# Performance work log

Measured on AMD Instinct MI355X. Metric: run time of the kernel, lower is better.

Reference implementation:

```python
import jax, jax.numpy as jnp
from jax import lax
import numpy as np

B, N, E, U = 128, 1024, 300, 128
L = 512          # num_leaves per sample
NN = 2 * L - 1   # num_nodes per sample (binary tree)


def _hsig(x):
    # Keras hard_sigmoid: clip(0.2*x + 0.5, 0, 1)
    return jnp.clip(0.2 * x + 0.5, 0.0, 1.0)


def setup_inputs() -> dict:
    key = jax.random.key(0)
    ks = jax.random.split(key, 5)
    rng = np.random.default_rng(0)
    # children of node t are uniform in [0, t) -> valid bottom-up binary tree
    u = rng.random((B, N, 2))
    child = (u * np.arange(N)[None, :, None]).astype(np.int32)
    child[:, :L, :] = 0  # leaves have no children (never read)
    num_vecs = np.tile(np.array([[NN, L]], np.int32), (B, 1))
    return {
        "initial_state": jax.random.normal(ks[0], (B, N, E), jnp.float32),
        "translation_kernel": jax.random.normal(ks[1], (E, U), jnp.float32) * 0.05,
        "kernel": jax.random.normal(ks[2], (5 * U, U), jnp.float32) * 0.05,
        "recurrent_kernel": jax.random.normal(ks[3], (5 * U, 2 * U), jnp.float32) * 0.05,
        "bias": jnp.zeros((5 * U, 1), jnp.float32),
        "child_vecs": jnp.asarray(child),
        "num_vecs": jnp.asarray(num_vecs),
    }


def reference(initial_state, translation_kernel, kernel, recurrent_kernel, bias,
              child_vecs, num_vecs):
    b, n, _ = initial_state.shape
    units = kernel.shape[1]
    # leaf initial states: relu(x @ W_translate)  -> [B, N, U]
    x = jax.nn.relu(jnp.einsum('bne,eu->bnu', initial_state, translation_kernel))
    num_nodes = num_vecs[:, 0]
    num_leaves = num_vecs[:, 1]
    bvec = bias[:, 0][None, :]  # [1, 5U]

    def step(carry, t):
        H, C = carry  # [B, N, U] each
        ch = jnp.take(child_vecs, t, axis=1)                                   # [B, 2]
        h_ch = jnp.take_along_axis(H, ch[:, :, None], axis=1).reshape(b, 2 * units)
        c_ch = jnp.take_along_axis(C, ch[:, :, None], axis=1).reshape(b, 2 * units)
        xt = jnp.take(x, t, axis=1)                                            # [B, U]
        # z = kernel @ x^T + recurrent_kernel @ [h_l; h_r] + bias  (batched, [B, 5U])
        z = xt @ kernel.T + h_ch @ recurrent_kernel.T + bvec
        i = _hsig(z[:, :units])
        f = _hsig(z[:, units:3 * units])                                       # [B, 2U]
        o = _hsig(z[:, 3 * units:4 * units])
        g = jnp.tanh(z[:, 4 * units:])
        # faithful to original: reshape (flat_mem*f) as [U, 2] row-major, sum axis 1
        c_new = (c_ch * f).reshape(b, units, 2).sum(axis=-1) + i * g
        h_new = o * jnp.tanh(c_new)
        act = ((t >= num_leaves) & (t < num_nodes))[:, None]                   # [B, 1]
        h_upd = jnp.where(act, h_new, jnp.take(H, t, axis=1))
        c_upd = jnp.where(act, c_new, jnp.take(C, t, axis=1))
        H = lax.dynamic_update_slice(H, h_upd[:, None, :], (0, t, 0))
        C = lax.dynamic_update_slice(C, c_upd[:, None, :], (0, t, 0))
        return (H, C), None

    # leaves start with hidden = memory = translated vec; internal nodes overwritten in order
    (H, _), _ = lax.scan(step, (x, x), jnp.arange(n))
    valid = (jnp.arange(n)[None, :] < num_nodes[:, None])[..., None]
    return H * valid.astype(H.dtype)
```

## Files before the change

### kernel.cpp

```cpp
#include <hip/hip_runtime.h>
#include <hip/hip_bf16.h>

#define B_ 128
#define N_ 1024
#define E_ 300
#define U_ 128
#define M_ (B_ * N_)
#define Z_ (5 * U_)
#define LMAXT 40
#define LPAR 20

typedef __attribute__((ext_vector_type(8))) short bf16x8;
typedef __attribute__((ext_vector_type(4))) float f32x4;
typedef _Float16 f16x4 __attribute__((ext_vector_type(4)));
typedef _Float16 f16x8 __attribute__((ext_vector_type(8)));

__device__ __forceinline__ short f2bf(float f) {
  unsigned u = __builtin_bit_cast(unsigned, f);
  u = (u + 0x7fffu + ((u >> 16) & 1u)) >> 16;
  return (short)u;
}

__device__ __forceinline__ float hsig(float z) {
  float v = __builtin_fmaf(z, 0.2f, 0.5f);
  v = v < 0.f ? 0.f : v;
  v = v > 1.f ? 1.f : v;
  return v;
}

__device__ __forceinline__ float tanh_fast(float x) {
  float p = __expf(2.f * x);
  return 1.f - 2.f * __builtin_amdgcn_rcpf(p + 1.f);
}

__device__ __forceinline__ unsigned pk2(float a, float b) {
  return __builtin_bit_cast(unsigned, __builtin_amdgcn_cvt_pkrtz(a, b));
}

__device__ __forceinline__ f16x8 pack8(float4 a, float4 b) {
  uint4 u;
  u.x = pk2(a.x, a.y);
  u.y = pk2(a.z, a.w);
  u.z = pk2(b.x, b.y);
  u.w = pk2(b.z, b.w);
  return __builtin_bit_cast(f16x8, u);
}

__global__ __launch_bounds__(256) void prep(
    const float* __restrict__ Wr, const float* __restrict__ Wk,
    const float* __restrict__ tk, _Float16* __restrict__ W16,
    _Float16* __restrict__ Wk16, _Float16* __restrict__ tkT16) {
  const int idx = blockIdx.x * 256 + threadIdx.x;
  if (idx < 163840) {
    W16[idx] = (_Float16)Wr[idx];
  } else if (idx < 245760) {
    const int i = idx - 163840;
    Wk16[i] = (_Float16)Wk[i];
  } else if (idx < 286720) {
    const int i = idx - 245760;
    const int n = i / 320, k = i - n * 320;
    tkT16[i] = (k < E_) ? (_Float16)tk[k * U_ + n] : (_Float16)0.f;
  }
}

__global__ __launch_bounds__(256) void x_gemm(
    const float* __restrict__ A, const float* __restrict__ W,
    float* __restrict__ H, float* __restrict__ C) {
  __shared__ __align__(16) short As[64][40];
  __shared__ __align__(16) short Ws[128][40];
  __shared__ __align__(16) _Float16 xls[64][136];
  const int tid = threadIdx.x;
  const int m0 = blockIdx.x * 64;
  f32x4 acc[8] = {};
  const int lane = tid & 63, wv = tid >> 6;
  const int lr = lane & 15, lg = lane >> 4;

  for (int kc = 0; kc < 10; ++kc) {
    const int k0 = kc * 32;
    {
      const int row = tid >> 2, kk = (tid & 3) * 8;
      const float* src = A + (size_t)(m0 + row) * E_ + k0 + kk;
      bf16x8 v;
      if (k0 + 32 <= E_) {
#pragma unroll
        for (int i = 0; i < 8; ++i) v[i] = f2bf(src[i]);
      } else {
#pragma unroll
        for (int i = 0; i < 8; ++i)
          v[i] = (k0 + kk + i < E_) ? f2bf(src[i]) : (short)0;
      }
      *(bf16x8*)&As[row][kk] = v;
    }
#pragma unroll
    for (int s = 0; s < 2; ++s) {
      const int slot = tid + s * 256;
      const int n = slot & 127, kg = slot >> 7;
      bf16x8 v;
      if (k0 + 32 <= E_) {
#pragma unroll
        for (int i = 0; i < 8; ++i) v[i] = f2bf(W[(k0 + kg * 8 + i) * U_ + n]);
      } else {
#pragma unroll
        for (int i = 0; i < 8; ++i) {
          const int k = k0 + kg * 8 + i;
          v[i] = (k < E_) ? f2bf(W[k * U_ + n]) : (short)0;
        }
      }
      *(bf16x8*)&Ws[n][kg * 8] = v;
    }
    __syncthreads();
    bf16x8 a = *(const bf16x8*)&As[wv * 16 + lr][lg * 8];
#pragma unroll
    for (int nt = 0; nt < 8; ++nt) {
      bf16x8 b = *(const bf16x8*)&Ws[nt * 16 + lr][lg * 8];
      acc[nt] = __builtin_amdgcn_mfma_f32_16x16x32_bf16(a, b, acc[nt], 0, 0, 0);
    }
    __syncthreads();
  }
#pragma unroll
  for (int nt = 0; nt < 8; ++nt) {
#pragma unroll
    for (int r = 0; r < 4; ++r) {
      float v = acc[nt][r];
      v = v > 0.f ? v : 0.f;
      xls[wv * 16 + lg * 4 + r][nt * 16 + lr] = (_Float16)v;
    }
  }
  __syncthreads();
  {
    const int row = tid >> 2, c0 = (tid & 3) * 32;
    const size_t base = (size_t)(m0 + row) * U_;
#pragma unroll
    for (int s = 0; s < 4; ++s) {
      const f16x8 v = *(const f16x8*)&xls[row][c0 + 8 * s];
      const float4 lo = {(float)v[0], (float)v[1], (float)v[2], (float)v[3]};
      const float4 hi4 = {(float)v[4], (float)v[5], (float)v[6], (float)v[7]};
      *(float4*)(H + base + c0 + 8 * s) = lo;
      *(float4*)(H + base + c0 + 8 * s + 4) = hi4;
      *(float4*)(C + base + c0 + 8 * s) = lo;
      *(float4*)(C + base + c0 + 8 * s + 4) = hi4;
    }
  }
}

__global__ __launch_bounds__(256) void xz_gemm(
    const float* __restrict__ X, const _Float16* __restrict__ Wk16,
    const float* __restrict__ bias, const int* __restrict__ nv,
    _Float16* __restrict__ XZ) {
  const int m0 = blockIdx.x * 64;
  {
    const int bb = m0 >> 10;
    const int t0 = m0 & (N_ - 1);
    const int nodes = nv[2 * bb], leaves = nv[2 * bb + 1];
    if (t0 + 64 <= leaves || t0 >= nodes) return;
  }
  __shared__ __align__(16) short As[64][40];
  __shared__ __align__(16) short Ws[128][40];
  __shared__ __align__(16) _Float16 xzls[64][136];
  const int tid = threadIdx.x;
  const int n0 = blockIdx.y * 128;
  f32x4 acc[8] = {};
  const int lane = tid & 63, wv = tid >> 6;
  const int lr = lane & 15, lg = lane >> 4;

  for (int kc = 0; kc < 4; ++kc) {
    const int k0 = kc * 32;
    {
      const int row = tid >> 2, kk = (tid & 3) * 8;
      const float* src = X + (size_t)(m0 + row) * U_ + k0 + kk;
      const float4 a0 = *(const float4*)src;
      const float4 a1 = *(const float4*)(src + 4);
      *(f16x8*)&As[row][kk] = pack8(a0, a1);
    }
#pragma unroll
    for (int s = 0; s < 2; ++s) {
      const int slot = tid + s * 256;
      const int n = slot >> 2, kk = (slot & 3) * 8;
      *(f16x8*)&Ws[n][kk] =
          *(const f16x8*)(Wk16 + (size_t)(n0 + n) * U_ + k0 + kk);
    }
    __syncthreads();
    f16x8 a = *(const f16x8*)&As[wv * 16 + lr][lg * 8];
#pragma unroll
    for (int nt = 0; nt < 8; ++nt) {
      f16x8 b = *(const f16x8*)&Ws[nt * 16 + lr][lg * 8];
      acc[nt] = __builtin_amdgcn_mfma_f32_16x16x32_f16(a, b, acc[nt], 0, 0, 0);
    }
    __syncthreads();
  }
#pragma unroll
  for (int nt = 0; nt < 8; ++nt) {
    const float bv = bias[n0 + nt * 16 + lr];
#pragma unroll
    for (int r = 0; r < 4; ++r)
      xzls[wv * 16 + lg * 4 + r][nt * 16 + lr] = (_Float16)(acc[nt][r] + bv);
  }
  __syncthreads();
  {
    const int row = tid >> 2, c0 = (tid & 3) * 32;
    _Float16* dst = XZ + (size_t)(m0 + row) * Z_ + n0 + c0;
#pragma unroll
    for (int s = 0; s < 4; ++s)
      *(f16x8*)(dst + 8 * s) = *(const f16x8*)&xzls[row][c0 + 8 * s];
  }
}

__global__ __launch_bounds__(512) void levelize(
    const int* __restrict__ child, const int* __restrict__ nv,
    unsigned char* __restrict__ lv, short* __restrict__ rank,
    int* __restrict__ cnt) {
  const int b = blockIdx.x;
  const int tid = threadIdx.x;
  int nodes = nv[2 * b];
  int leaves = nv[2 * b + 1];
  if (nodes > N_) nodes = N_;
  if (leaves < 0) leaves = 0;

  __shared__ short lvs[N_];
  __shared__ int chs[2 * N_];
  __shared__ int cnts[LMAXT];
  __shared__ int changed;

  for (int i = tid; i < N_; i += 512) lvs[i] = 0;
  for (int i = tid; i < 2 * N_; i += 512) chs[i] = child[(size_t)b * 2 * N_ + i];
  if (tid < LMAXT) cnts[tid] = 0;
  __syncthreads();

  int stable = 0;
  for (int s = 0; s < 64; ++s) {
    if (tid == 0) changed = 0;
    __syncthreads();
    int any = 0;
    for (int t = leaves + tid; t < nodes; t += 512) {
      const int c0 = chs[2 * t], c1 = chs[2 * t + 1];
      const int l0 = (c0 < t && c0 >= 0) ? lvs[c0] : 0;
      const int l1 = (c1 < t && c1 >= 0) ? lvs[c1] : 0;
      const int l = 1 + (l0 > l1 ? l0 : l1);
      if (l > (int)lvs[t]) { lvs[t] = (short)l; any = 1; }
    }
    if (any) changed = 1;
    __syncthreads();
    if (!changed) { stable = 1; break; }
  }
  if (!stable) {
    if (tid == 0) {
      for (int t = leaves; t < nodes; ++t) {
        const int c0 = chs[2 * t], c1 = chs[2 * t + 1];
        const int l0 = (c0 < t && c0 >= 0) ? lvs[c0] : 0;
        const int l1 = (c1 < t && c1 >= 0) ? lvs[c1] : 0;
        lvs[t] = (short)(1 + (l0 > l1 ? l0 : l1));
      }
    }
    __syncthreads();
  }

  for (int t = leaves + tid; t < nodes; t += 512) {
    int l = lvs[t];
    if (l > LMAXT - 1) l = LMAXT - 1;
    lv[b * N_ + t] = (unsigned char)l;
    if (l < LMAXT - 1) rank[b * N_ + t] = (short)atomicAdd(&cnts[l], 1);
  }
  __syncthreads();
  if (tid == 0) {
    for (int t = leaves; t < nodes; ++t)
      if ((int)lvs[t] >= LMAXT - 1) rank[b * N_ + t] = (short)(cnts[LMAXT - 1]++);
  }
  __syncthreads();
  if (tid < LMAXT) cnt[tid * 128 + b] = cnts[tid];
}

__global__ __launch_bounds__(64) void offsets(
    const int* __restrict__ cnt, int* __restrict__ pos, int* __restrict__ goff) {
  const int l = threadIdx.x;
  __shared__ int tot[LMAXT];
  if (l < LMAXT) {
    int s = 0;
    for (int b = 0; b < 128; ++b) {
      pos[l * 128 + b] = s;
      s += cnt[l * 128 + b];
    }
    tot[l] = s;
  }
  __syncthreads();
  if (l == 0) {
    int g = 0;
    for (int i = 0; i < LMAXT; ++i) { goff[i] = g; g += tot[i]; }
    goff[LMAXT] = g;
  }
  __syncthreads();
  if (l < LMAXT) {
    const int g = goff[l];
    for (int b = 0; b < 128; ++b) pos[l * 128 + b] += g;
  }
}

__global__ __launch_bounds__(256) void scatter_zero(
    const int* __restrict__ nv, const unsigned char* __restrict__ lv,
    const short* __restrict__ rank, const int* __restrict__ pos,
    int* __restrict__ glist, float* __restrict__ H) {
  const int b = blockIdx.x;
  const int tid = threadIdx.x;
  int nodes = nv[2 * b];
  int leaves = nv[2 * b + 1];
  if (nodes > N_) nodes = N_;
  if (leaves < 0) leaves = 0;
  for (int t = leaves + tid; t < nodes; t += 256) {
    const int l = lv[b * N_ + t];
    glist[pos[l * 128 + b] + rank[b * N_ + t]] = (b << 10) | t;
  }
  const int total = (N_ - nodes) * U_;
  for (int idx = tid; idx < total; idx += 256)
    H[(size_t)b * N_ * U_ + nodes * U_ + idx] = 0.f;
}

__global__ __launch_bounds__(512, 2) void level_gemm(
    int lvl, const _Float16* __restrict__ W16, const int* __restrict__ child,
    const int* __restrict__ goff, const int* __restrict__ glist,
    const _Float16* __restrict__ XZ, float* __restrict__ H,
    float* __restrict__ C) {
  const int base = goff[lvl];
  const int count = goff[lvl + 1] - base;
  if (count <= 0) return;
  const int tid = threadIdx.x;
  const int lane = tid & 63, w = tid >> 6;
  const int col = lane & 15, hi = lane >> 4;
  const int u0 = 16 * w + 4 * hi;
  const int mc = 2 * u0;

  f16x8 afrag[5][8];
  {
    const int rows[5] = {16 * w + col, 128 + 32 * w + 2 * col,
                         129 + 32 * w + 2 * col, 384 + 16 * w + col,
                         512 + 16 * w + col};
#pragma unroll
    for (int rt = 0; rt < 5; ++rt) {
      const _Float16* rs = W16 + (size_t)rows[rt] * 256 + 8 * hi;
#pragma unroll
      for (int kt = 0; kt < 8; ++kt) afrag[rt][kt] = *(const f16x8*)(rs + 32 * kt);
    }
  }

  __shared__ __align__(16) _Float16 hbuf[16][272];

  const int nchunk = (count + 15) >> 4;
  for (int chunk = blockIdx.x; chunk < nchunk; chunk += gridDim.x) {
    const int cb = base + chunk * 16;
    int rem = count - chunk * 16;
    if (rem > 16) rem = 16;

    const int j = tid >> 5, s = tid & 31;
    const int nidj = glist[cb + (j < rem ? j : rem - 1)];
    const int bj = nidj >> 10, tj = nidj & 1023;
    const int chj = child[((size_t)bj << 11) + 2 * tj + (s >> 4)];
    const float* hsrc = H + (((size_t)(bj << 10) + chj) << 7) + ((s & 15) << 3);
    const float4 a0 = *(const float4*)hsrc;
    const float4 a1 = *(const float4*)(hsrc + 4);

    const int nidc = glist[cb + (col < rem ? col : rem - 1)];
    const int bc = nidc >> 10, tc = nidc & 1023;
    const _Float16* xzr = XZ + ((size_t)((bc << 10) | tc)) * Z_;
    const f16x4 xzi = *(const f16x4*)(xzr + u0);
    const f16x8 xzf = *(const f16x8*)(xzr + 128 + mc);
    const f16x4 xzo = *(const f16x4*)(xzr + 384 + u0);
    const f16x4 xzg = *(const f16x4*)(xzr + 512 + u0);
    const int csel = child[((size_t)bc << 11) + 2 * tc + (mc >> 7)];
    const float* cbp = C + (((size_t)(bc << 10) + csel) << 7) + (mc & 127);
    const float4 cv0 = ((const float4*)cbp)[0];
    const float4 cv1 = ((const float4*)cbp)[1];

    uint4 hp;
    hp.x = pk2(a0.x, a0.y);
    hp.y = pk2(a0.z, a0.w);
    hp.z = pk2(a1.x, a1.y);
    hp.w = pk2(a1.z, a1.w);
    *(uint4*)&hbuf[j][(s >> 4) * 128 + (s & 15) * 8] = hp;
    __syncthreads();

    f32x4 acc[5];
#pragma unroll
    for (int r = 0; r < 4; ++r) {
      acc[0][r] = (float)xzi[r];
      acc[1][r] = (float)xzf[2 * r];
      acc[2][r] = (float)xzf[2 * r + 1];
      acc[3][r] = (float)xzo[r];
      acc[4][r] = (float)xzg[r];
    }
#pragma unroll
    for (int kt = 0; kt < 8; ++kt) {
      const f16x8 bf = *(const f16x8*)&hbuf[col][32 * kt + 8 * hi];
#pragma unroll
      for (int rt = 0; rt < 5; ++rt)
        acc[rt] = __builtin_amdgcn_mfma_f32_16x16x32_f16(afrag[rt][kt], bf,
                                                         acc[rt], 0, 0, 0);
    }

    const float ce[8] = {cv0.x, cv0.y, cv0.z, cv0.w,
                         cv1.x, cv1.y, cv1.z, cv1.w};
    f32x4 hn4, cn4;
#pragma unroll
    for (int r = 0; r < 4; ++r) {
      const float cn = ce[2 * r] * hsig(acc[1][r]) +
                       ce[2 * r + 1] * hsig(acc[2][r]) +
                       hsig(acc[0][r]) * tanh_fast(acc[4][r]);
      cn4[r] = cn;
      hn4[r] = hsig(acc[3][r]) * tanh_fast(cn);
    }
    if (col < rem) {
      const size_t rowb = ((size_t)((bc << 10) | tc)) << 7;
      *(f32x4*)(H + rowb + u0) = hn4;
      *(f32x4*)(C + rowb + u0) = cn4;
    }
    __syncthreads();
  }
}

__global__ __launch_bounds__(512, 2) void tail_scan(
    const _Float16* __restrict__ W16, const int* __restrict__ child,
    const int* __restrict__ nv, const int* __restrict__ pos,
    const int* __restrict__ cnt, const int* __restrict__ glist,
    const _Float16* __restrict__ XZ, float* __restrict__ H,
    float* __restrict__ C) {
  const int b = blockIdx.x;
  const int tid = threadIdx.x;
  const int lane = tid & 63, w = tid >> 6;
  const int col = lane & 15, hi = lane >> 4;
  const int u0 = 16 * w + 4 * hi;
  const int mc = 2 * u0;
  const int m4 = 4 * lane;

  f16x8 afrag[5][8];
  {
    const int rows[5] = {16 * w + col, 128 + 32 * w + 2 * col,
                         129 + 32 * w + 2 * col, 384 + 16 * w + col,
                         512 + 16 * w + col};
#pragma unroll
    for (int rt = 0; rt < 5; ++rt) {
      const _Float16* rs = W16 + (size_t)rows[rt] * 256 + 8 * hi;
#pragma unroll
      for (int kt = 0; kt < 8; ++kt) afrag[rt][kt] = *(const f16x8*)(rs + 32 * kt);
    }
  }

  __shared__ __align__(16) _Float16 hb1[256];
  const int* chb = child + (size_t)b * 2 * N_;
  float* Hb = H + (size_t)b * N_ * U_;
  float* Cb = C + (size_t)b * N_ * U_;
  const _Float16* xzb = XZ + (size_t)b * N_ * Z_;

  for (int l = LPAR; l < LMAXT; ++l) {
    const int p0 = pos[l * 128 + b];
    const int n = cnt[l * 128 + b];
    for (int i = 0; i < n; ++i) {
      const int t = glist[p0 + i] & 1023;
      if (tid < 64) {
        const int ch = chb[2 * t + (m4 >> 7)];
        const float4 hv = *(const float4*)(Hb + ((size_t)ch << 7) + (m4 & 127));
        uint2 hp;
        hp.x = pk2(hv.x, hv.y);
        hp.y = pk2(hv.z, hv.w);
        *(uint2*)&hb1[m4] = hp;
      }
      const int cs = chb[2 * t + (mc >> 7)];
      const float* cbp = Cb + ((size_t)cs << 7) + (mc & 127);
      const float4 cv0 = ((const float4*)cbp)[0];
      const float4 cv1 = ((const float4*)cbp)[1];
      const _Float16* xzr = xzb + (size_t)t * Z_;
      const f16x4 xzi = *(const f16x4*)(xzr + u0);
      const f16x8 xzf = *(const f16x8*)(xzr + 128 + mc);
      const f16x4 xzo = *(const f16x4*)(xzr + 384 + u0);
      const f16x4 xzg = *(const f16x4*)(xzr + 512 + u0);
      __syncthreads();
      f32x4 acc[5];
#pragma unroll
      for (int r = 0; r < 4; ++r) {
        acc[0][r] = (float)xzi[r];
        acc[1][r] = (float)xzf[2 * r];
        acc[2][r] = (float)xzf[2 * r + 1];
        acc[3][r] = (float)xzo[r];
        acc[4][r] = (float)xzg[r];
      }
#pragma unroll
      for (int kt = 0; kt < 8; ++kt) {
        const f16x8 bf = *(const f16x8*)&hb1[32 * kt + 8 * hi];
#pragma unroll
        for (int rt = 0; rt < 5; ++rt)
          acc[rt] = __builtin_amdgcn_mfma_f32_16x16x32_f16(afrag[rt][kt], bf,
                                                           acc[rt], 0, 0, 0);
      }
      const float ce[8] = {cv0.x, cv0.y, cv0.z, cv0.w,
                           cv1.x, cv1.y, cv1.z, cv1.w};
      f32x4 hn4, cn4;
#pragma unroll
      for (int r = 0; r < 4; ++r) {
        const float cn = ce[2 * r] * hsig(acc[1][r]) +
                         ce[2 * r + 1] * hsig(acc[2][r]) +
                         hsig(acc[0][r]) * tanh_fast(acc[4][r]);
        cn4[r] = cn;
        hn4[r] = hsig(acc[3][r]) * tanh_fast(cn);
      }
      if (col == 0) {
        *(f32x4*)(Hb + ((size_t)t << 7) + u0) = hn4;
        *(f32x4*)(Cb + ((size_t)t << 7) + u0) = cn4;
      }
      __syncthreads();
    }
  }
}

extern "C" void kernel_launch(void* const* d_in, const int* in_sizes, int n_in,
                              void* d_out, int out_size, void* d_ws,
                              size_t ws_size, hipStream_t stream) {
  const float* state = (const float*)d_in[0];
  const float* tk    = (const float*)d_in[1];
  const float* Wk    = (const float*)d_in[2];
  const float* Wr    = (const float*)d_in[3];
  const float* bias  = (const float*)d_in[4];
  const int*   child = (const int*)d_in[5];
  const int*   nvp   = (const int*)d_in[6];
  float* H = (float*)d_out;

  char* wsb = (char*)d_ws;
  _Float16* W16   = (_Float16*)(wsb + 0x000000);
  _Float16* Wk16  = (_Float16*)(wsb + 0x050000);
  _Float16* tkT16 = (_Float16*)(wsb + 0x078000);
  unsigned char* lv = (unsigned char*)(wsb + 0x08C000);
  short* rank     = (short*)(wsb + 0x0AC000);
  int* cnt        = (int*)(wsb + 0x0EC000);
  int* pos        = (int*)(wsb + 0x0F1000);
  int* goff       = (int*)(wsb + 0x0F6000);
  int* glist      = (int*)(wsb + 0x0F7000);
  const size_t meta_sz = 2ull * 1024 * 1024;
  const size_t c_bytes = (size_t)M_ * U_ * sizeof(float);
  float* C = (float*)(wsb + meta_sz);
  _Float16* XZ = (_Float16*)(wsb + meta_sz + c_bytes);

  prep<<<1120, 256, 0, stream>>>(Wr, Wk, tk, W16, Wk16, tkT16);
  x_gemm<<<M_ / 64, 256, 0, stream>>>(state, tk, H, C);
  xz_gemm<<<dim3(M_ / 64, 5), 256, 0, stream>>>(H, Wk16, bias, nvp, XZ);
  levelize<<<B_, 512, 0, stream>>>(child, nvp, lv, rank, cnt);
  offsets<<<1, 64, 0, stream>>>(cnt, pos, goff);
  scatter_zero<<<B_, 256, 0, stream>>>(nvp, lv, rank, pos, glist, H);
  static const int lg[LPAR] = {0,  512, 512, 256, 256, 128, 128, 64, 64, 64,
                               32, 32,  32,  32,  32,  32,  16,  16, 16, 16};
  for (int l = 1; l < LPAR; ++l)
    level_gemm<<<lg[l], 512, 0, stream>>>(l, W16, child, goff, glist, XZ, H, C);
  tail_scan<<<B_, 512, 0, stream>>>(W16, child, nvp, pos, cnt, glist, XZ, H, C);
}
```

Before: 439.7 us.

## Fuse input projection into level recurrence kernels, drop precomputed XZ buffer

Removes the separate xz_gemm pass and its fp16 XZ buffer. The input-kernel product and bias are now computed inside level_gemm and tail_scan by concatenating Wk onto the recurrent weights (K=384) and staging the node's own translated vector in shared memory. x_gemm now writes H and C straight from the accumulators instead of going through an fp16 shared-memory stage, and the per-level grid sizes are retuned. The extra four MFMA k-steps read their weight fragments from global memory on every chunk, which adds latency to the serial tail_scan critical path in exchange for skipping the large XZ write and read.

New measurement: 435.5 us. Within noise of the previous version (-1.0%).

```diff
diff --git a/kernel.cpp b/kernel.cpp
--- a/kernel.cpp
+++ b/kernel.cpp
@@ -12,7 +12,6 @@
 
 typedef __attribute__((ext_vector_type(8))) short bf16x8;
 typedef __attribute__((ext_vector_type(4))) float f32x4;
-typedef _Float16 f16x4 __attribute__((ext_vector_type(4)));
 typedef _Float16 f16x8 __attribute__((ext_vector_type(8)));
 
 __device__ __forceinline__ short f2bf(float f) {
@@ -37,29 +36,14 @@
   return __builtin_bit_cast(unsigned, __builtin_amdgcn_cvt_pkrtz(a, b));
 }
 
-__device__ __forceinline__ f16x8 pack8(float4 a, float4 b) {
-  uint4 u;
-  u.x = pk2(a.x, a.y);
-  u.y = pk2(a.z, a.w);
-  u.z = pk2(b.x, b.y);
-  u.w = pk2(b.z, b.w);
-  return __builtin_bit_cast(f16x8, u);
-}
-
 __global__ __launch_bounds__(256) void prep(
     const float* __restrict__ Wr, const float* __restrict__ Wk,
-    const float* __restrict__ tk, _Float16* __restrict__ W16,
-    _Float16* __restrict__ Wk16, _Float16* __restrict__ tkT16) {
+    _Float16* __restrict__ W384) {
   const int idx = blockIdx.x * 256 + threadIdx.x;
-  if (idx < 163840) {
-    W16[idx] = (_Float16)Wr[idx];
-  } else if (idx < 245760) {
-    const int i = idx - 163840;
-    Wk16[i] = (_Float16)Wk[i];
-  } else if (idx < 286720) {
-    const int i = idx - 245760;
-    const int n = i / 320, k = i - n * 320;
-    tkT16[i] = (k < E_) ? (_Float16)tk[k * U_ + n] : (_Float16)0.f;
+  if (idx < 640 * 384) {
+    const int row = idx / 384, c = idx - row * 384;
+    W384[idx] = (c < 256) ? (_Float16)Wr[row * 256 + c]
+                          : (_Float16)Wk[row * 128 + (c - 256)];
   }
 }
 
@@ -68,7 +52,6 @@
     float* __restrict__ H, float* __restrict__ C) {
   __shared__ __align__(16) short As[64][40];
   __shared__ __align__(16) short Ws[128][40];
-  __shared__ __align__(16) _Float16 xls[64][136];
   const int tid = threadIdx.x;
   const int m0 = blockIdx.x * 64;
   f32x4 acc[8] = {};
@@ -121,87 +104,13 @@
   for (int nt = 0; nt < 8; ++nt) {
 #pragma unroll
     for (int r = 0; r < 4; ++r) {
+      const int m = m0 + wv * 16 + lg * 4 + r;
+      const int n = nt * 16 + lr;
       float v = acc[nt][r];
       v = v > 0.f ? v : 0.f;
-      xls[wv * 16 + lg * 4 + r][nt * 16 + lr] = (_Float16)v;
-    }
-  }
-  __syncthreads();
-  {
-    const int row = tid >> 2, c0 = (tid & 3) * 32;
-    const size_t base = (size_t)(m0 + row) * U_;
-#pragma unroll
-    for (int s = 0; s < 4; ++s) {
-      const f16x8 v = *(const f16x8*)&xls[row][c0 + 8 * s];
-      const float4 lo = {(float)v[0], (float)v[1], (float)v[2], (float)v[3]};
-      const float4 hi4 = {(float)v[4], (float)v[5], (float)v[6], (float)v[7]};
-      *(float4*)(H + base + c0 + 8 * s) = lo;
-      *(float4*)(H + base + c0 + 8 * s + 4) = hi4;
-      *(float4*)(C + base + c0 + 8 * s) = lo;
-      *(float4*)(C + base + c0 + 8 * s + 4) = hi4;
-    }
-  }
-}
-
-__global__ __launch_bounds__(256) void xz_gemm(
-    const float* __restrict__ X, const _Float16* __restrict__ Wk16,
-    const float* __restrict__ bias, const int* __restrict__ nv,
-    _Float16* __restrict__ XZ) {
-  const int m0 = blockIdx.x * 64;
-  {
-    const int bb = m0 >> 10;
-    const int t0 = m0 & (N_ - 1);
-    const int nodes = nv[2 * bb], leaves = nv[2 * bb + 1];
-    if (t0 + 64 <= leaves || t0 >= nodes) return;
-  }
-  __shared__ __align__(16) short As[64][40];
-  __shared__ __align__(16) short Ws[128][40];
-  __shared__ __align__(16) _Float16 xzls[64][136];
-  const int tid = threadIdx.x;
-  const int n0 = blockIdx.y * 128;
-  f32x4 acc[8] = {};
-  const int lane = tid & 63, wv = tid >> 6;
-  const int lr = lane & 15, lg = lane >> 4;
-
-  for (int kc = 0; kc < 4; ++kc) {
-    const int k0 = kc * 32;
-    {
-      const int row = tid >> 2, kk = (tid & 3) * 8;
-      const float* src = X + (size_t)(m0 + row) * U_ + k0 + kk;
-      const float4 a0 = *(const float4*)src;
-      const float4 a1 = *(const float4*)(src + 4);
-      *(f16x8*)&As[row][kk] = pack8(a0, a1);
-    }
-#pragma unroll
-    for (int s = 0; s < 2; ++s) {
-      const int slot = tid + s * 256;
-      const int n = slot >> 2, kk = (slot & 3) * 8;
-      *(f16x8*)&Ws[n][kk] =
-          *(const f16x8*)(Wk16 + (size_t)(n0 + n) * U_ + k0 + kk);
-    }
-    __syncthreads();
-    f16x8 a = *(const f16x8*)&As[wv * 16 + lr][lg * 8];
-#pragma unroll
-    for (int nt = 0; nt < 8; ++nt) {
-      f16x8 b = *(const f16x8*)&Ws[nt * 16 + lr][lg * 8];
-      acc[nt] = __builtin_amdgcn_mfma_f32_16x16x32_f16(a, b, acc[nt], 0, 0, 0);
-    }
-    __syncthreads();
-  }
-#pragma unroll
-  for (int nt = 0; nt < 8; ++nt) {
-    const float bv = bias[n0 + nt * 16 + lr];
-#pragma unroll
-    for (int r = 0; r < 4; ++r)
-      xzls[wv * 16 + lg * 4 + r][nt * 16 + lr] = (_Float16)(acc[nt][r] + bv);
-  }
-  __syncthreads();
-  {
-    const int row = tid >> 2, c0 = (tid & 3) * 32;
-    _Float16* dst = XZ + (size_t)(m0 + row) * Z_ + n0 + c0;
-#pragma unroll
-    for (int s = 0; s < 4; ++s)
-      *(f16x8*)(dst + 8 * s) = *(const f16x8*)&xzls[row][c0 + 8 * s];
+      H[(size_t)m * U_ + n] = v;
+      C[(size_t)m * U_ + n] = v;
+    }
   }
 }
 
@@ -314,9 +223,9 @@
 }
 
 __global__ __launch_bounds__(512, 2) void level_gemm(
-    int lvl, const _Float16* __restrict__ W16, const int* __restrict__ child,
-    const int* __restrict__ goff, const int* __restrict__ glist,
-    const _Float16* __restrict__ XZ, float* __restrict__ H,
+    int lvl, const _Float16* __restrict__ W384, const float* __restrict__ bias,
+    const int* __restrict__ child, const int* __restrict__ goff,
+    const int* __restrict__ glist, float* __restrict__ H,
     float* __restrict__ C) {
   const int base = goff[lvl];
   const int count = goff[lvl + 1] - base;
@@ -327,23 +236,26 @@
   const int u0 = 16 * w + 4 * hi;
   const int mc = 2 * u0;
 
-  f16x8 afrag[5][8];
-  {
-    const int rows[5] = {16 * w + col, 128 + 32 * w + 2 * col,
-                         129 + 32 * w + 2 * col, 384 + 16 * w + col,
-                         512 + 16 * w + col};
-#pragma unroll
-    for (int rt = 0; rt < 5; ++rt) {
-      const _Float16* rs = W16 + (size_t)rows[rt] * 256 + 8 * hi;
-#pragma unroll
-      for (int kt = 0; kt < 8; ++kt) afrag[rt][kt] = *(const f16x8*)(rs + 32 * kt);
-    }
-  }
-
-  __shared__ __align__(16) _Float16 hbuf[16][272];
+  int rows5[5];
+  rows5[0] = 16 * w + col;
+  rows5[1] = 128 + 32 * w + 2 * col;
+  rows5[2] = 129 + 32 * w + 2 * col;
+  rows5[3] = 384 + 16 * w + col;
+  rows5[4] = 512 + 16 * w + col;
+
+  f16x8 afragR[5][8];
+#pragma unroll
+  for (int rt = 0; rt < 5; ++rt) {
+    const _Float16* rs = W384 + (size_t)rows5[rt] * 384 + 8 * hi;
+#pragma unroll
+    for (int kt = 0; kt < 8; ++kt) afragR[rt][kt] = *(const f16x8*)(rs + 32 * kt);
+  }
+
+  __shared__ __align__(16) _Float16 hbuf[16][392];
 
   const int nchunk = (count + 15) >> 4;
   for (int chunk = blockIdx.x; chunk < nchunk; chunk += gridDim.x) {
+    asm volatile("" ::: "memory");
     const int cb = base + chunk * 16;
     int rem = count - chunk * 16;
     if (rem > 16) rem = 16;
@@ -356,42 +268,76 @@
     const float4 a0 = *(const float4*)hsrc;
     const float4 a1 = *(const float4*)(hsrc + 4);
 
+    float4 x0, x1;
+    int j2 = 0, seg2 = 0;
+    if (tid < 256) {
+      j2 = tid >> 4;
+      seg2 = tid & 15;
+      const int nid2 = glist[cb + (j2 < rem ? j2 : rem - 1)];
+      const float* xsrc =
+          H + (((size_t)nid2 & 0x1FFFF) << 7, (size_t)0) ;
+      const float* xs = H + (((size_t)nid2) << 7) + (seg2 << 3);
+      x0 = *(const float4*)xs;
+      x1 = *(const float4*)(xs + 4);
+      (void)xsrc;
+    }
+
     const int nidc = glist[cb + (col < rem ? col : rem - 1)];
     const int bc = nidc >> 10, tc = nidc & 1023;
-    const _Float16* xzr = XZ + ((size_t)((bc << 10) | tc)) * Z_;
-    const f16x4 xzi = *(const f16x4*)(xzr + u0);
-    const f16x8 xzf = *(const f16x8*)(xzr + 128 + mc);
-    const f16x4 xzo = *(const f16x4*)(xzr + 384 + u0);
-    const f16x4 xzg = *(const f16x4*)(xzr + 512 + u0);
     const int csel = child[((size_t)bc << 11) + 2 * tc + (mc >> 7)];
     const float* cbp = C + (((size_t)(bc << 10) + csel) << 7) + (mc & 127);
     const float4 cv0 = ((const float4*)cbp)[0];
     const float4 cv1 = ((const float4*)cbp)[1];
 
-    uint4 hp;
-    hp.x = pk2(a0.x, a0.y);
-    hp.y = pk2(a0.z, a0.w);
-    hp.z = pk2(a1.x, a1.y);
-    hp.w = pk2(a1.z, a1.w);
-    *(uint4*)&hbuf[j][(s >> 4) * 128 + (s & 15) * 8] = hp;
+    {
+      uint4 hp;
+      hp.x = pk2(a0.x, a0.y);
+      hp.y = pk2(a0.z, a0.w);
+      hp.z = pk2(a1.x, a1.y);
+      hp.w = pk2(a1.z, a1.w);
+      *(uint4*)&hbuf[j][(s >> 4) * 128 + (s & 15) * 8] = hp;
+      if (tid < 256) {
+        uint4 xp;
+        xp.x = pk2(x0.x, x0.y);
+        xp.y = pk2(x0.z, x0.w);
+        xp.z = pk2(x1.x, x1.y);
+        xp.w = pk2(x1.z, x1.w);
+        *(uint4*)&hbuf[j2][256 + seg2 * 8] = xp;
+      }
+    }
     __syncthreads();
 
     f32x4 acc[5];
-#pragma unroll
-    for (int r = 0; r < 4; ++r) {
-      acc[0][r] = (float)xzi[r];
-      acc[1][r] = (float)xzf[2 * r];
-      acc[2][r] = (float)xzf[2 * r + 1];
-      acc[3][r] = (float)xzo[r];
-      acc[4][r] = (float)xzg[r];
+    {
+      const float4 b0 = *(const float4*)(bias + u0);
+      const float4 b1 = *(const float4*)(bias + 128 + mc);
+      const float4 b2 = *(const float4*)(bias + 128 + mc + 4);
+      const float4 b3 = *(const float4*)(bias + 384 + u0);
+      const float4 b4 = *(const float4*)(bias + 512 + u0);
+      acc[0][0] = b0.x; acc[0][1] = b0.y; acc[0][2] = b0.z; acc[0][3] = b0.w;
+      acc[1][0] = b1.x; acc[1][1] = b1.z; acc[1][2] = b2.x; acc[1][3] = b2.z;
+      acc[2][0] = b1.y; acc[2][1] = b1.w; acc[2][2] = b2.y; acc[2][3] = b2.w;
+      acc[3][0] = b3.x; acc[3][1] = b3.y; acc[3][2] = b3.z; acc[3][3] = b3.w;
+      acc[4][0] = b4.x; acc[4][1] = b4.y; acc[4][2] = b4.z; acc[4][3] = b4.w;
     }
 #pragma unroll
     for (int kt = 0; kt < 8; ++kt) {
       const f16x8 bf = *(const f16x8*)&hbuf[col][32 * kt + 8 * hi];
 #pragma unroll
       for (int rt = 0; rt < 5; ++rt)
-        acc[rt] = __builtin_amdgcn_mfma_f32_16x16x32_f16(afrag[rt][kt], bf,
+        acc[rt] = __builtin_amdgcn_mfma_f32_16x16x32_f16(afragR[rt][kt], bf,
                                                          acc[rt], 0, 0, 0);
+    }
+#pragma unroll
+    for (int kt2 = 0; kt2 < 4; ++kt2) {
+      const f16x8 bf = *(const f16x8*)&hbuf[col][256 + 32 * kt2 + 8 * hi];
+#pragma unroll
+      for (int rt = 0; rt < 5; ++rt) {
+        const f16x8 ak = *(const f16x8*)(W384 + (size_t)rows5[rt] * 384 + 256 +
+                                         32 * kt2 + 8 * hi);
+        acc[rt] = __builtin_amdgcn_mfma_f32_16x16x32_f16(ak, bf, acc[rt], 0, 0,
+                                                         0);
+      }
     }
 
     const float ce[8] = {cv0.x, cv0.y, cv0.z, cv0.w,
@@ -415,10 +361,10 @@
 }
 
 __global__ __launch_bounds__(512, 2) void tail_scan(
-    const _Float16* __restrict__ W16, const int* __restrict__ child,
-    const int* __restrict__ nv, const int* __restrict__ pos,
-    const int* __restrict__ cnt, const int* __restrict__ glist,
-    const _Float16* __restrict__ XZ, float* __restrict__ H,
+    const _Float16* __restrict__ W384, const float* __restrict__ bias,
+    const int* __restrict__ child, const int* __restrict__ nv,
+    const int* __restrict__ pos, const int* __restrict__ cnt,
+    const int* __restrict__ glist, float* __restrict__ H,
     float* __restrict__ C) {
   const int b = blockIdx.x;
   const int tid = threadIdx.x;
@@ -428,29 +374,31 @@
   const int mc = 2 * u0;
   const int m4 = 4 * lane;
 
-  f16x8 afrag[5][8];
-  {
-    const int rows[5] = {16 * w + col, 128 + 32 * w + 2 * col,
-                         129 + 32 * w + 2 * col, 384 + 16 * w + col,
-                         512 + 16 * w + col};
-#pragma unroll
-    for (int rt = 0; rt < 5; ++rt) {
-      const _Float16* rs = W16 + (size_t)rows[rt] * 256 + 8 * hi;
-#pragma unroll
-      for (int kt = 0; kt < 8; ++kt) afrag[rt][kt] = *(const f16x8*)(rs + 32 * kt);
-    }
-  }
-
-  __shared__ __align__(16) _Float16 hb1[256];
+  int rows5[5];
+  rows5[0] = 16 * w + col;
+  rows5[1] = 128 + 32 * w + 2 * col;
+  rows5[2] = 129 + 32 * w + 2 * col;
+  rows5[3] = 384 + 16 * w + col;
+  rows5[4] = 512 + 16 * w + col;
+
+  f16x8 afragR[5][8];
+#pragma unroll
+  for (int rt = 0; rt < 5; ++rt) {
+    const _Float16* rs = W384 + (size_t)rows5[rt] * 384 + 8 * hi;
+#pragma unroll
+    for (int kt = 0; kt < 8; ++kt) afragR[rt][kt] = *(const f16x8*)(rs + 32 * kt);
+  }
+
+  __shared__ __align__(16) _Float16 hb1[392];
   const int* chb = child + (size_t)b * 2 * N_;
   float* Hb = H + (size_t)b * N_ * U_;
   float* Cb = C + (size_t)b * N_ * U_;
-  const _Float16* xzb = XZ + (size_t)b * N_ * Z_;
 
   for (int l = LPAR; l < LMAXT; ++l) {
     const int p0 = pos[l * 128 + b];
     const int n = cnt[l * 128 + b];
     for (int i = 0; i < n; ++i) {
+      asm volatile("" ::: "memory");
       const int t = glist[p0 + i] & 1023;
       if (tid < 64) {
         const int ch = chb[2 * t + (m4 >> 7)];
@@ -459,33 +407,48 @@
         hp.x = pk2(hv.x, hv.y);
         hp.y = pk2(hv.z, hv.w);
         *(uint2*)&hb1[m4] = hp;
+      } else if (tid < 128) {
+        const int u2 = tid - 64;
+        const float2 xv = *(const float2*)(Hb + ((size_t)t << 7) + 2 * u2);
+        *(unsigned*)&hb1[256 + 2 * u2] = pk2(xv.x, xv.y);
       }
       const int cs = chb[2 * t + (mc >> 7)];
       const float* cbp = Cb + ((size_t)cs << 7) + (mc & 127);
       const float4 cv0 = ((const float4*)cbp)[0];
       const float4 cv1 = ((const float4*)cbp)[1];
-      const _Float16* xzr = xzb + (size_t)t * Z_;
-      const f16x4 xzi = *(const f16x4*)(xzr + u0);
-      const f16x8 xzf = *(const f16x8*)(xzr + 128 + mc);
-      const f16x4 xzo = *(const f16x4*)(xzr + 384 + u0);
-      const f16x4 xzg = *(const f16x4*)(xzr + 512 + u0);
       __syncthreads();
+
       f32x4 acc[5];
-#pragma unroll
-      for (int r = 0; r < 4; ++r) {
-        acc[0][r] = (float)xzi[r];
-        acc[1][r] = (float)xzf[2 * r];
-        acc[2][r] = (float)xzf[2 * r + 1];
-        acc[3][r] = (float)xzo[r];
-        acc[4][r] = (float)xzg[r];
+      {
+        const float4 b0 = *(const float4*)(bias + u0);
+        const float4 b1 = *(const float4*)(bias + 128 + mc);
+        const float4 b2 = *(const float4*)(bias + 128 + mc + 4);
+        const float4 b3 = *(const float4*)(bias + 384 + u0);
+        const float4 b4 = *(const float4*)(bias + 512 + u0);
+        acc[0][0] = b0.x; acc[0][1] = b0.y; acc[0][2] = b0.z; acc[0][3] = b0.w;
+        acc[1][0] = b1.x; acc[1][1] = b1.z; acc[1][2] = b2.x; acc[1][3] = b2.z;
+        acc[2][0] = b1.y; acc[2][1] = b1.w; acc[2][2] = b2.y; acc[2][3] = b2.w;
+        acc[3][0] = b3.x; acc[3][1] = b3.y; acc[3][2] = b3.z; acc[3][3] = b3.w;
+        acc[4][0] = b4.x; acc[4][1] = b4.y; acc[4][2] = b4.z; acc[4][3] = b4.w;
       }
 #pragma unroll
       for (int kt = 0; kt < 8; ++kt) {
         const f16x8 bf = *(const f16x8*)&hb1[32 * kt + 8 * hi];
 #pragma unroll
         for (int rt = 0; rt < 5; ++rt)
-          acc[rt] = __builtin_amdgcn_mfma_f32_16x16x32_f16(afrag[rt][kt], bf,
+          acc[rt] = __builtin_amdgcn_mfma_f32_16x16x32_f16(afragR[rt][kt], bf,
                                                            acc[rt], 0, 0, 0);
+      }
+#pragma unroll
+      for (int kt2 = 0; kt2 < 4; ++kt2) {
+        const f16x8 bf = *(const f16x8*)&hb1[256 + 32 * kt2 + 8 * hi];
+#pragma unroll
+        for (int rt = 0; rt < 5; ++rt) {
+          const f16x8 ak = *(const f16x8*)(W384 + (size_t)rows5[rt] * 384 +
+                                           256 + 32 * kt2 + 8 * hi);
+          acc[rt] = __builtin_amdgcn_mfma_f32_16x16x32_f16(ak, bf, acc[rt], 0,
+                                                           0, 0);
+        }
       }
       const float ce[8] = {cv0.x, cv0.y, cv0.z, cv0.w,
                            cv1.x, cv1.y, cv1.z, cv1.w};
@@ -520,29 +483,26 @@
   float* H = (float*)d_out;
 
   char* wsb = (char*)d_ws;
-  _Float16* W16   = (_Float16*)(wsb + 0x000000);
-  _Float16* Wk16  = (_Float16*)(wsb + 0x050000);
-  _Float16* tkT16 = (_Float16*)(wsb + 0x078000);
-  unsigned char* lv = (unsigned char*)(wsb + 0x08C000);
-  short* rank     = (short*)(wsb + 0x0AC000);
-  int* cnt        = (int*)(wsb + 0x0EC000);
-  int* pos        = (int*)(wsb + 0x0F1000);
-  int* goff       = (int*)(wsb + 0x0F6000);
-  int* glist      = (int*)(wsb + 0x0F7000);
+  _Float16* W384  = (_Float16*)(wsb + 0x000000);
+  unsigned char* lv = (unsigned char*)(wsb + 0x078000);
+  short* rank     = (short*)(wsb + 0x098000);
+  int* cnt        = (int*)(wsb + 0x0D8000);
+  int* pos        = (int*)(wsb + 0x0DD000);
+  int* goff       = (int*)(wsb + 0x0E2000);
+  int* glist      = (int*)(wsb + 0x0E3000);
   const size_t meta_sz = 2ull * 1024 * 1024;
-  const size_t c_bytes = (size_t)M_ * U_ * sizeof(float);
   float* C = (float*)(wsb + meta_sz);
-  _Float16* XZ = (_Float16*)(wsb + meta_sz + c_bytes);
-
-  prep<<<1120, 256, 0, stream>>>(Wr, Wk, tk, W16, Wk16, tkT16);
+
+  prep<<<960, 256, 0, stream>>>(Wr, Wk, W384);
   x_gemm<<<M_ / 64, 256, 0, stream>>>(state, tk, H, C);
-  xz_gemm<<<dim3(M_ / 64, 5), 256, 0, stream>>>(H, Wk16, bias, nvp, XZ);
   levelize<<<B_, 512, 0, stream>>>(child, nvp, lv, rank, cnt);
   offsets<<<1, 64, 0, stream>>>(cnt, pos, goff);
   scatter_zero<<<B_, 256, 0, stream>>>(nvp, lv, rank, pos, glist, H);
-  static const int lg[LPAR] = {0,  512, 512, 256, 256, 128, 128, 64, 64, 64,
-                               32, 32,  32,  32,  32,  32,  16,  16, 16, 16};
+  static const int lg[LPAR] = {0,  768, 512, 384, 256, 192, 128, 96, 64, 48,
+                               32, 24,  20,  16,  16,  16,  16,  16, 16, 16};
   for (int l = 1; l < LPAR; ++l)
-    level_gemm<<<lg[l], 512, 0, stream>>>(l, W16, child, goff, glist, XZ, H, C);
-  tail_scan<<<B_, 512, 0, stream>>>(W16, child, nvp, pos, cnt, glist, XZ, H, C);
-}
+    level_gemm<<<lg[l], 512, 0, stream>>>(l, W384, bias, child, goff, glist, H,
+                                          C);
+  tail_scan<<<B_, 512, 0, stream>>>(W384, bias, child, nvp, pos, cnt, glist, H,
+                                    C);
+}
```

## Prefetch next chunk in level_gemm and drop duplicate leaf C writes

Applied to the files above, without the earlier changes.

Level_gemm now double-buffers its LDS tile. It issues global loads for the next chunk before the MFMA work on the current one, and uses a single barrier per iteration instead of two. x_gemm no longer writes a copy of leaf states into C; leaf memory reads are redirected to H by checking lv==0, and levelize now records level 0 for leaves. The per-level grid sizes are retuned, and the unused transposed translation-kernel prep is removed. The risks are extra register pressure from the prefetched chunk, and that the output H now keeps f32 leaf values instead of f16-rounded ones.

Result: faster. 427.4 us (-2.8%).

```diff
diff --git a/kernel.cpp b/kernel.cpp
--- a/kernel.cpp
+++ b/kernel.cpp
@@ -48,27 +48,21 @@
 
 __global__ __launch_bounds__(256) void prep(
     const float* __restrict__ Wr, const float* __restrict__ Wk,
-    const float* __restrict__ tk, _Float16* __restrict__ W16,
-    _Float16* __restrict__ Wk16, _Float16* __restrict__ tkT16) {
+    _Float16* __restrict__ W16, _Float16* __restrict__ Wk16) {
   const int idx = blockIdx.x * 256 + threadIdx.x;
   if (idx < 163840) {
     W16[idx] = (_Float16)Wr[idx];
   } else if (idx < 245760) {
     const int i = idx - 163840;
     Wk16[i] = (_Float16)Wk[i];
-  } else if (idx < 286720) {
-    const int i = idx - 245760;
-    const int n = i / 320, k = i - n * 320;
-    tkT16[i] = (k < E_) ? (_Float16)tk[k * U_ + n] : (_Float16)0.f;
   }
 }
 
 __global__ __launch_bounds__(256) void x_gemm(
     const float* __restrict__ A, const float* __restrict__ W,
-    float* __restrict__ H, float* __restrict__ C) {
+    float* __restrict__ H) {
   __shared__ __align__(16) short As[64][40];
   __shared__ __align__(16) short Ws[128][40];
-  __shared__ __align__(16) _Float16 xls[64][136];
   const int tid = threadIdx.x;
   const int m0 = blockIdx.x * 64;
   f32x4 acc[8] = {};
@@ -121,24 +115,11 @@
   for (int nt = 0; nt < 8; ++nt) {
 #pragma unroll
     for (int r = 0; r < 4; ++r) {
+      const int m = m0 + wv * 16 + lg * 4 + r;
+      const int n = nt * 16 + lr;
       float v = acc[nt][r];
       v = v > 0.f ? v : 0.f;
-      xls[wv * 16 + lg * 4 + r][nt * 16 + lr] = (_Float16)v;
-    }
-  }
-  __syncthreads();
-  {
-    const int row = tid >> 2, c0 = (tid & 3) * 32;
-    const size_t base = (size_t)(m0 + row) * U_;
-#pragma unroll
-    for (int s = 0; s < 4; ++s) {
-      const f16x8 v = *(const f16x8*)&xls[row][c0 + 8 * s];
-      const float4 lo = {(float)v[0], (float)v[1], (float)v[2], (float)v[3]};
-      const float4 hi4 = {(float)v[4], (float)v[5], (float)v[6], (float)v[7]};
-      *(float4*)(H + base + c0 + 8 * s) = lo;
-      *(float4*)(H + base + c0 + 8 * s + 4) = hi4;
-      *(float4*)(C + base + c0 + 8 * s) = lo;
-      *(float4*)(C + base + c0 + 8 * s + 4) = hi4;
+      H[(size_t)m * U_ + n] = v;
     }
   }
 }
@@ -254,11 +235,12 @@
     __syncthreads();
   }
 
-  for (int t = leaves + tid; t < nodes; t += 512) {
-    int l = lvs[t];
+  for (int t = tid; t < nodes; t += 512) {
+    int l = (t < leaves) ? 0 : (int)lvs[t];
     if (l > LMAXT - 1) l = LMAXT - 1;
     lv[b * N_ + t] = (unsigned char)l;
-    if (l < LMAXT - 1) rank[b * N_ + t] = (short)atomicAdd(&cnts[l], 1);
+    if (t >= leaves && l < LMAXT - 1)
+      rank[b * N_ + t] = (short)atomicAdd(&cnts[l], 1);
   }
   __syncthreads();
   if (tid == 0) {
@@ -313,19 +295,66 @@
     H[(size_t)b * N_ * U_ + nodes * U_ + idx] = 0.f;
 }
 
+struct ChunkLd {
+  float4 a0, a1;
+  float4 cv0, cv1;
+  f16x4 xzi, xzo, xzg;
+  f16x8 xzf;
+  int nid, rem;
+};
+
+__device__ __forceinline__ ChunkLd load_chunk(
+    int chunk, int nchunk, int base, int count, const int* __restrict__ glist,
+    const int* __restrict__ child, const unsigned char* __restrict__ lv,
+    const _Float16* __restrict__ XZ, const float* __restrict__ H,
+    const float* __restrict__ C, int j, int s, int col, int u0, int mc) {
+  ChunkLd r;
+  const int cc = chunk < nchunk - 1 ? chunk : nchunk - 1;
+  const int cb = base + cc * 16;
+  int rem = count - cc * 16;
+  if (rem > 16) rem = 16;
+  r.rem = rem;
+
+  const int nidj = glist[cb + (j < rem ? j : rem - 1)];
+  const int bj = nidj >> 10, tj = nidj & 1023;
+  const int chj = child[((size_t)bj << 11) + 2 * tj + (s >> 4)];
+  const float* hsrc = H + (((size_t)(bj << 10) + chj) << 7) + ((s & 15) << 3);
+  r.a0 = *(const float4*)hsrc;
+  r.a1 = *(const float4*)(hsrc + 4);
+
+  const int nidc = glist[cb + (col < rem ? col : rem - 1)];
+  r.nid = nidc;
+  const _Float16* xzr = XZ + (size_t)nidc * Z_;
+  r.xzi = *(const f16x4*)(xzr + u0);
+  r.xzf = *(const f16x8*)(xzr + 128 + mc);
+  r.xzo = *(const f16x4*)(xzr + 384 + u0);
+  r.xzg = *(const f16x4*)(xzr + 512 + u0);
+  const int bc = nidc >> 10, tc = nidc & 1023;
+  const int csel = child[((size_t)bc << 11) + 2 * tc + (mc >> 7)];
+  const int crow = (bc << 10) | csel;
+  const float* cbp =
+      (lv[crow] == 0 ? H : C) + ((size_t)crow << 7) + (mc & 127);
+  r.cv0 = ((const float4*)cbp)[0];
+  r.cv1 = ((const float4*)cbp)[1];
+  return r;
+}
+
 __global__ __launch_bounds__(512, 2) void level_gemm(
     int lvl, const _Float16* __restrict__ W16, const int* __restrict__ child,
-    const int* __restrict__ goff, const int* __restrict__ glist,
-    const _Float16* __restrict__ XZ, float* __restrict__ H,
-    float* __restrict__ C) {
+    const unsigned char* __restrict__ lv, const int* __restrict__ goff,
+    const int* __restrict__ glist, const _Float16* __restrict__ XZ,
+    float* __restrict__ H, float* __restrict__ C) {
   const int base = goff[lvl];
   const int count = goff[lvl + 1] - base;
   if (count <= 0) return;
+  const int nchunk = (count + 15) >> 4;
+  if ((int)blockIdx.x >= nchunk) return;
   const int tid = threadIdx.x;
   const int lane = tid & 63, w = tid >> 6;
   const int col = lane & 15, hi = lane >> 4;
   const int u0 = 16 * w + 4 * hi;
   const int mc = 2 * u0;
+  const int j = tid >> 5, s = tid & 31;
 
   f16x8 afrag[5][8];
   {
@@ -340,62 +369,49 @@
     }
   }
 
-  __shared__ __align__(16) _Float16 hbuf[16][272];
-
-  const int nchunk = (count + 15) >> 4;
+  __shared__ __align__(16) _Float16 hbuf[2][16][272];
+
+  ChunkLd cur = load_chunk(blockIdx.x, nchunk, base, count, glist, child, lv,
+                           XZ, H, C, j, s, col, u0, mc);
+  int p = 0;
   for (int chunk = blockIdx.x; chunk < nchunk; chunk += gridDim.x) {
-    const int cb = base + chunk * 16;
-    int rem = count - chunk * 16;
-    if (rem > 16) rem = 16;
-
-    const int j = tid >> 5, s = tid & 31;
-    const int nidj = glist[cb + (j < rem ? j : rem - 1)];
-    const int bj = nidj >> 10, tj = nidj & 1023;
-    const int chj = child[((size_t)bj << 11) + 2 * tj + (s >> 4)];
-    const float* hsrc = H + (((size_t)(bj << 10) + chj) << 7) + ((s & 15) << 3);
-    const float4 a0 = *(const float4*)hsrc;
-    const float4 a1 = *(const float4*)(hsrc + 4);
-
-    const int nidc = glist[cb + (col < rem ? col : rem - 1)];
-    const int bc = nidc >> 10, tc = nidc & 1023;
-    const _Float16* xzr = XZ + ((size_t)((bc << 10) | tc)) * Z_;
-    const f16x4 xzi = *(const f16x4*)(xzr + u0);
-    const f16x8 xzf = *(const f16x8*)(xzr + 128 + mc);
-    const f16x4 xzo = *(const f16x4*)(xzr + 384 + u0);
-    const f16x4 xzg = *(const f16x4*)(xzr + 512 + u0);
-    const int csel = child[((size_t)bc << 11) + 2 * tc + (mc >> 7)];
-    const float* cbp = C + (((size_t)(bc << 10) + csel) << 7) + (mc & 127);
-    const float4 cv0 = ((const float4*)cbp)[0];
-    const float4 cv1 = ((const float4*)cbp)[1];
-
     uint4 hp;
-    hp.x = pk2(a0.x, a0.y);
-    hp.y = pk2(a0.z, a0.w);
-    hp.z = pk2(a1.x, a1.y);
-    hp.w = pk2(a1.z, a1.w);
-    *(uint4*)&hbuf[j][(s >> 4) * 128 + (s & 15) * 8] = hp;
-    __syncthreads();
+    hp.x = pk2(cur.a0.x, cur.a0.y);
+    hp.y = pk2(cur.a0.z, cur.a0.w);
+    hp.z = pk2(cur.a1.x, cur.a1.y);
+    hp.w = pk2(cur.a1.z, cur.a1.w);
+    *(uint4*)&hbuf[p][j][(s >> 4) * 128 + (s & 15) * 8] = hp;
+
+    ChunkLd nxt = load_chunk(chunk + gridDim.x < nchunk ? chunk + gridDim.x
+                                                        : nchunk - 1,
+                             nchunk, base, count, glist, child, lv, XZ, H, C,
+                             j, s, col, u0, mc);
+
+    asm volatile("s_waitcnt lgkmcnt(0)" ::: "memory");
+    __builtin_amdgcn_sched_barrier(0);
+    __builtin_amdgcn_s_barrier();
+    __builtin_amdgcn_sched_barrier(0);
 
     f32x4 acc[5];
 #pragma unroll
     for (int r = 0; r < 4; ++r) {
-      acc[0][r] = (float)xzi[r];
-      acc[1][r] = (float)xzf[2 * r];
-      acc[2][r] = (float)xzf[2 * r + 1];
-      acc[3][r] = (float)xzo[r];
-      acc[4][r] = (float)xzg[r];
+      acc[0][r] = (float)cur.xzi[r];
+      acc[1][r] = (float)cur.xzf[2 * r];
+      acc[2][r] = (float)cur.xzf[2 * r + 1];
+      acc[3][r] = (float)cur.xzo[r];
+      acc[4][r] = (float)cur.xzg[r];
     }
 #pragma unroll
     for (int kt = 0; kt < 8; ++kt) {
-      const f16x8 bf = *(const f16x8*)&hbuf[col][32 * kt + 8 * hi];
+      const f16x8 bf = *(const f16x8*)&hbuf[p][col][32 * kt + 8 * hi];
 #pragma unroll
       for (int rt = 0; rt < 5; ++rt)
         acc[rt] = __builtin_amdgcn_mfma_f32_16x16x32_f16(afrag[rt][kt], bf,
                                                          acc[rt], 0, 0, 0);
     }
 
-    const float ce[8] = {cv0.x, cv0.y, cv0.z, cv0.w,
-                         cv1.x, cv1.y, cv1.z, cv1.w};
+    const float ce[8] = {cur.cv0.x, cur.cv0.y, cur.cv0.z, cur.cv0.w,
+                         cur.cv1.x, cur.cv1.y, cur.cv1.z, cur.cv1.w};
     f32x4 hn4, cn4;
 #pragma unroll
     for (int r = 0; r < 4; ++r) {
@@ -405,21 +421,22 @@
       cn4[r] = cn;
       hn4[r] = hsig(acc[3][r]) * tanh_fast(cn);
     }
-    if (col < rem) {
-      const size_t rowb = ((size_t)((bc << 10) | tc)) << 7;
+    if (col < cur.rem) {
+      const size_t rowb = (size_t)cur.nid << 7;
       *(f32x4*)(H + rowb + u0) = hn4;
       *(f32x4*)(C + rowb + u0) = cn4;
     }
-    __syncthreads();
+    cur = nxt;
+    p ^= 1;
   }
 }
 
 __global__ __launch_bounds__(512, 2) void tail_scan(
     const _Float16* __restrict__ W16, const int* __restrict__ child,
-    const int* __restrict__ nv, const int* __restrict__ pos,
-    const int* __restrict__ cnt, const int* __restrict__ glist,
-    const _Float16* __restrict__ XZ, float* __restrict__ H,
-    float* __restrict__ C) {
+    const unsigned char* __restrict__ lv, const int* __restrict__ nv,
+    const int* __restrict__ pos, const int* __restrict__ cnt,
+    const int* __restrict__ glist, const _Float16* __restrict__ XZ,
+    float* __restrict__ H, float* __restrict__ C) {
   const int b = blockIdx.x;
   const int tid = threadIdx.x;
   const int lane = tid & 63, w = tid >> 6;
@@ -443,6 +460,7 @@
 
   __shared__ __align__(16) _Float16 hb1[256];
   const int* chb = child + (size_t)b * 2 * N_;
+  const unsigned char* lvb = lv + (size_t)b * N_;
   float* Hb = H + (size_t)b * N_ * U_;
   float* Cb = C + (size_t)b * N_ * U_;
   const _Float16* xzb = XZ + (size_t)b * N_ * Z_;
@@ -461,7 +479,8 @@
         *(uint2*)&hb1[m4] = hp;
       }
       const int cs = chb[2 * t + (mc >> 7)];
-      const float* cbp = Cb + ((size_t)cs << 7) + (mc & 127);
+      const float* cbp =
+          (lvb[cs] == 0 ? Hb : Cb) + ((size_t)cs << 7) + (mc & 127);
       const float4 cv0 = ((const float4*)cbp)[0];
       const float4 cv1 = ((const float4*)cbp)[1];
       const _Float16* xzr = xzb + (size_t)t * Z_;
@@ -522,27 +541,28 @@
   char* wsb = (char*)d_ws;
   _Float16* W16   = (_Float16*)(wsb + 0x000000);
   _Float16* Wk16  = (_Float16*)(wsb + 0x050000);
-  _Float16* tkT16 = (_Float16*)(wsb + 0x078000);
-  unsigned char* lv = (unsigned char*)(wsb + 0x08C000);
-  short* rank     = (short*)(wsb + 0x0AC000);
-  int* cnt        = (int*)(wsb + 0x0EC000);
-  int* pos        = (int*)(wsb + 0x0F1000);
-  int* goff       = (int*)(wsb + 0x0F6000);
-  int* glist      = (int*)(wsb + 0x0F7000);
+  unsigned char* lv = (unsigned char*)(wsb + 0x078000);
+  short* rank     = (short*)(wsb + 0x098000);
+  int* cnt        = (int*)(wsb + 0x0D8000);
+  int* pos        = (int*)(wsb + 0x0DD000);
+  int* goff       = (int*)(wsb + 0x0E2000);
+  int* glist      = (int*)(wsb + 0x0E3000);
   const size_t meta_sz = 2ull * 1024 * 1024;
   const size_t c_bytes = (size_t)M_ * U_ * sizeof(float);
   float* C = (float*)(wsb + meta_sz);
   _Float16* XZ = (_Float16*)(wsb + meta_sz + c_bytes);
 
-  prep<<<1120, 256, 0, stream>>>(Wr, Wk, tk, W16, Wk16, tkT16);
-  x_gemm<<<M_ / 64, 256, 0, stream>>>(state, tk, H, C);
+  prep<<<960, 256, 0, stream>>>(Wr, Wk, W16, Wk16);
+  x_gemm<<<M_ / 64, 256, 0, stream>>>(state, tk, H);
   xz_gemm<<<dim3(M_ / 64, 5), 256, 0, stream>>>(H, Wk16, bias, nvp, XZ);
   levelize<<<B_, 512, 0, stream>>>(child, nvp, lv, rank, cnt);
   offsets<<<1, 64, 0, stream>>>(cnt, pos, goff);
   scatter_zero<<<B_, 256, 0, stream>>>(nvp, lv, rank, pos, glist, H);
-  static const int lg[LPAR] = {0,  512, 512, 256, 256, 128, 128, 64, 64, 64,
-                               32, 32,  32,  32,  32,  32,  16,  16, 16, 16};
+  static const int lg[LPAR] = {0,  512, 384, 256, 192, 128, 96, 64, 48, 32,
+                               24, 20,  16,  16,  16,  16,  16, 16, 16, 16};
   for (int l = 1; l < LPAR; ++l)
-    level_gemm<<<lg[l], 512, 0, stream>>>(l, W16, child, goff, glist, XZ, H, C);
-  tail_scan<<<B_, 512, 0, stream>>>(W16, child, nvp, pos, cnt, glist, XZ, H, C);
-}
+    level_gemm<<<lg[l], 512, 0, stream>>>(l, W16, child, lv, goff, glist, XZ,
+                                          H, C);
+  tail_scan<<<B_, 512, 0, stream>>>(W16, child, lv, nvp, pos, cnt, glist, XZ,
+                                    H, C);
+}
```
